# Kernel tuning notes

Hardware: AMD Instinct MI355X
Metric: run time of the kernel (lower is better)

## Reference

```python
import jax, jax.numpy as jnp
import numpy as np

B, A, DV, RNN, H = 256, 196, 2048, 1024, 512

def setup_inputs() -> dict:
    key = jax.random.key(0)
    ks = jax.random.split(key, 8)
    s = lambda d: 1.0 / np.sqrt(d)
    return {
        "h_att": jax.random.normal(ks[0], (B, RNN), jnp.float32),
        "prev_h2": jax.random.normal(ks[1], (B, RNN), jnp.float32),
        "imgs_features": jax.random.normal(ks[2], (B, A, DV), jnp.float32),
        "W_v": jax.random.normal(ks[3], (DV, H), jnp.float32) * s(DV),
        "b_v": jnp.zeros((H,), jnp.float32),
        "W_ha": jax.random.normal(ks[4], (RNN, H), jnp.float32) * s(RNN),
        "b_ha": jnp.zeros((H,), jnp.float32),
        "W_hv": jax.random.normal(ks[5], (RNN, H), jnp.float32) * s(RNN),
        "b_hv": jnp.zeros((H,), jnp.float32),
        "W_f": jax.random.normal(ks[6], (H, 1), jnp.float32) * s(H),
        "b_f": jnp.zeros((1,), jnp.float32),
    }

def reference(h_att, prev_h2, imgs_features, W_v, b_v, W_ha, b_ha, W_hv, b_hv, W_f, b_f):
    # project image regions: [B, A, H]
    p_imgs = jnp.einsum('bad,dh->bah', imgs_features, W_v) + b_v
    # project hidden states: [B, H] -> broadcast over regions
    att_hatt = h_att @ W_ha + b_ha          # [B, H]
    att_hvis = prev_h2 @ W_hv + b_hv        # [B, H]
    dot = p_imgs + att_hatt[:, None, :] + att_hvis[:, None, :]  # [B, A, H]
    # dropout is identity in eval mode
    att = (jax.nn.relu(dot) @ W_f)[..., 0] + b_f[0]  # [B, A]
    alpha = jax.nn.softmax(att, axis=1)              # [B, A]
    # weighted sum over regions -> [B, 2048]
    return jnp.einsum('bad,ba->bd', imgs_features, alpha)
```

## Files before the change

kernel.cpp:

```cpp
#include <hip/hip_runtime.h>
#include <stdint.h>

typedef float f32x4 __attribute__((ext_vector_type(4)));
typedef short s16x8 __attribute__((ext_vector_type(8)));
typedef unsigned u32x2 __attribute__((ext_vector_type(2)));

#define B_SZ 256
#define A_RG 196
#define DVD  2048
#define RNN  1024
#define H_SZ 512
#define NKT  (DVD / 32)

__device__ __forceinline__ unsigned short f2bf(float f) {
    unsigned u = __builtin_bit_cast(unsigned, f);
    u = u + 0x7FFFu + ((u >> 16) & 1u);
    return (unsigned short)(u >> 16);
}

__device__ __forceinline__ unsigned cvt2(float a, float b) {
    unsigned r;
    asm("v_cvt_pk_bf16_f32 %0, %1, %2" : "=v"(r) : "v"(a), "v"(b));
    return r;
}

__global__ __launch_bounds__(256) void k_prepW(const float* __restrict__ Wv,
                                               unsigned short* __restrict__ Wt4) {
    __shared__ float tile[64][65];
    int kb = blockIdx.x >> 3, ct = blockIdx.x & 7;
    int k0 = kb * 64, c0 = ct * 64;
    int t = threadIdx.x;
    int cl = t & 63, rq = t >> 6;
#pragma unroll
    for (int i = 0; i < 16; ++i) {
        int r = rq * 16 + i;
        tile[r][cl] = Wv[(size_t)(k0 + r) * H_SZ + c0 + cl];
    }
    __syncthreads();
    int kl = t & 63;
#pragma unroll
    for (int i = 0; i < 16; ++i) {
        int cr = rq * 16 + i;
        int col = c0 + cr;
        int k = k0 + kl;
        int f = col >> 4, lr = col & 15;
        int kt = k >> 5, g = (k >> 3) & 3, e = k & 7;
        size_t dst = ((size_t)(kt * 32 + f) * 64 + g * 16 + lr) * 8 + e;
        Wt4[dst] = f2bf(tile[kl][cr]);
    }
}

__global__ __launch_bounds__(256) void k_base(const float* __restrict__ h_att,
                                              const float* __restrict__ prev_h2,
                                              const float* __restrict__ W_ha,
                                              const float* __restrict__ b_ha,
                                              const float* __restrict__ W_hv,
                                              const float* __restrict__ b_hv,
                                              const float* __restrict__ b_v,
                                              float* __restrict__ base_g) {
    __shared__ float ha_s[4][RNN];
    __shared__ float pv_s[4][RNN];
    int bg = blockIdx.x >> 2, hg = blockIdx.x & 3;
    int t = threadIdx.x;
#pragma unroll
    for (int i = 0; i < 16; ++i) {
        int idx = i * 256 + t;
        int bl = idx >> 10, k = idx & 1023;
        ha_s[bl][k] = h_att[(size_t)(bg * 4 + bl) * RNN + k];
        pv_s[bl][k] = prev_h2[(size_t)(bg * 4 + bl) * RNN + k];
    }
    __syncthreads();
    int h = hg * 128 + (t & 127);
    int br = t >> 7;
    float aA0 = 0, aA1 = 0, aV0 = 0, aV1 = 0;
#pragma unroll 4
    for (int k = 0; k < RNN; ++k) {
        float w1 = W_ha[(size_t)k * H_SZ + h];
        float w2 = W_hv[(size_t)k * H_SZ + h];
        aA0 = fmaf(ha_s[br * 2][k],     w1, aA0);
        aA1 = fmaf(ha_s[br * 2 + 1][k], w1, aA1);
        aV0 = fmaf(pv_s[br * 2][k],     w2, aV0);
        aV1 = fmaf(pv_s[br * 2 + 1][k], w2, aV1);
    }
    float bias = b_ha[h] + b_hv[h] + b_v[h];
    base_g[(size_t)(bg * 4 + br * 2) * H_SZ + h]     = aA0 + aV0 + bias;
    base_g[(size_t)(bg * 4 + br * 2 + 1) * H_SZ + h] = aA1 + aV1 + bias;
}

__global__ __launch_bounds__(1024, 4) void k_fused(const float* __restrict__ imgs,
                                                   const unsigned short* __restrict__ Wt4,
                                                   const float* __restrict__ base_g,
                                                   const float* __restrict__ W_f,
                                                   float* __restrict__ out) {
    __shared__ __align__(16) short A_s[2][128 * 32];
    __shared__ float att_part[8][128];
    __shared__ float e_s[128];
    __shared__ float scal_r;
    __shared__ float scal_l;

    const int b = blockIdx.x;
    const int t = threadIdx.x;
    const int lane = t & 63, w = t >> 6;
    const int wm = w >> 3, wn = w & 7;
    const int lr = lane & 15, g = lane >> 4;

    const float* imgb = imgs + (size_t)b * A_RG * DVD;
    const char* Bp = (const char*)Wt4 + ((size_t)(wn * 4) * 64 + lane) * 16;

    f32x4 o2;
    float o0 = 0.f, o1 = 0.f;
    float m_run = -1e30f, l_run = 0.f;
    (void)o2;

    const int arow = t >> 3, ac = t & 7;
    const unsigned awr = (unsigned)(arow * 64 +
        ((((ac >> 1) ^ ((arow ^ (arow >> 2)) & 3)) << 4) | ((ac & 1) << 3)));

    unsigned ard[4];
#pragma unroll
    for (int mf = 0; mf < 4; ++mf) {
        int r = wm * 64 + mf * 16 + lr;
        ard[mf] = (unsigned)(r * 64 + ((g ^ ((r ^ (r >> 2)) & 3)) << 4));
    }

    for (int at = 0; at < 2; ++at) {
        const bool last = (at == 1);
        const int m0 = at * 128;

        const float* Ag = imgb + (size_t)min(m0 + arow, A_RG - 1) * DVD + ac * 4;

        f32x4 acc[4][4] = {};
        f32x4 rA;
        s16x8 aF[4], bR[4];

        auto ldA = [&](int kt) {
            rA = *(const f32x4*)(Ag + (size_t)kt * 32);
        };
        auto wrA = [&](int buf) {
            u32x2 pk;
            pk[0] = cvt2(rA[0], rA[1]);
            pk[1] = cvt2(rA[2], rA[3]);
            *(u32x2*)((char*)A_s[buf] + awr) = pk;
        };
        auto ldB = [&](int kt) {
            const char* p = Bp + (size_t)kt * 32768;
#pragma unroll
            for (int n = 0; n < 4; ++n)
                bR[n] = *(const s16x8*)(p + n * 1024);
        };

        ldB(0);
        ldA(0);
        wrA(0);
        asm volatile("s_waitcnt lgkmcnt(0)" ::: "memory");
        __builtin_amdgcn_sched_barrier(0);
        __builtin_amdgcn_s_barrier();

        for (int kt = 0; kt < NKT; ++kt) {
            if (kt + 1 < NKT) ldA(kt + 1);
            const char* Ac = (const char*)A_s[kt & 1];
#pragma unroll
            for (int mf = 0; mf < 4; ++mf)
                aF[mf] = *(const s16x8*)(Ac + ard[mf]);
            __builtin_amdgcn_s_setprio(1);
#pragma unroll
            for (int mf = 0; mf < 4; ++mf)
#pragma unroll
                for (int n = 0; n < 4; ++n)
                    acc[mf][n] = __builtin_amdgcn_mfma_f32_16x16x32_bf16(
                        aF[mf], bR[n], acc[mf][n], 0, 0, 0);
            __builtin_amdgcn_s_setprio(0);
            if (kt + 1 < NKT) {
                ldB(kt + 1);
                wrA((kt + 1) & 1);
                asm volatile("s_waitcnt lgkmcnt(0)" ::: "memory");
                __builtin_amdgcn_sched_barrier(0);
                __builtin_amdgcn_s_barrier();
            }
        }

        {
            float wfv[4], bs[4];
#pragma unroll
            for (int n = 0; n < 4; ++n) {
                int col = wn * 64 + n * 16 + lr;
                wfv[n] = W_f[col];
                bs[n] = base_g[(size_t)b * H_SZ + col];
            }
#pragma unroll
            for (int mf = 0; mf < 4; ++mf) {
                float pj[4] = {0.f, 0.f, 0.f, 0.f};
#pragma unroll
                for (int n = 0; n < 4; ++n) {
                    float a0 = fmaxf(acc[mf][n][0] + bs[n], 0.f);
                    float a1 = fmaxf(acc[mf][n][1] + bs[n], 0.f);
                    float a2 = fmaxf(acc[mf][n][2] + bs[n], 0.f);
                    float a3 = fmaxf(acc[mf][n][3] + bs[n], 0.f);
                    pj[0] = fmaf(a0, wfv[n], pj[0]);
                    pj[1] = fmaf(a1, wfv[n], pj[1]);
                    pj[2] = fmaf(a2, wfv[n], pj[2]);
                    pj[3] = fmaf(a3, wfv[n], pj[3]);
                }
#pragma unroll
                for (int j = 0; j < 4; ++j) {
                    float s = pj[j];
                    s += __shfl_xor(s, 1);
                    s += __shfl_xor(s, 2);
                    s += __shfl_xor(s, 4);
                    s += __shfl_xor(s, 8);
                    if (lr == 0)
                        att_part[wn][wm * 64 + mf * 16 + g * 4 + j] = s;
                }
            }
        }
        __builtin_amdgcn_s_barrier();

        if (w == 0) {
            int gr0 = m0 + lane, gr1 = m0 + lane + 64;
            float s0, s1;
            {
                float a = 0.f, c = 0.f;
#pragma unroll
                for (int q = 0; q < 8; ++q) {
                    a += att_part[q][lane];
                    c += att_part[q][lane + 64];
                }
                s0 = (gr0 < A_RG) ? a : -1e30f;
                s1 = (gr1 < A_RG) ? c : -1e30f;
            }
            float mx = fmaxf(s0, s1);
            for (int d = 1; d < 64; d <<= 1) mx = fmaxf(mx, __shfl_xor(mx, d));
            float m_new = fmaxf(m_run, mx);
            float r = __expf(m_run - m_new);
            float e0 = __expf(s0 - m_new);
            float e1 = __expf(s1 - m_new);
            float es = e0 + e1;
            for (int d = 1; d < 64; d <<= 1) es += __shfl_xor(es, d);
            l_run = l_run * r + es;
            m_run = m_new;
            e_s[lane] = e0;
            e_s[lane + 64] = e1;
            if (lane == 0) {
                scal_r = r;
                if (last) scal_l = l_run;
            }
        }
        __builtin_amdgcn_s_barrier();

        {
            float r = scal_r;
            o0 *= r; o1 *= r;
            const float2* vb = (const float2*)imgb + t;
            const int AV = last ? (A_RG - 128) : 128;
#pragma unroll 4
            for (int a = 0; a < AV; ++a) {
                float e = e_s[a];
                float2 v = vb[(size_t)(m0 + a) * (DVD / 2)];
                o0 = fmaf(e, v.x, o0);
                o1 = fmaf(e, v.y, o1);
            }
        }
    }

    float linv = 1.0f / scal_l;
    float2 res = make_float2(o0 * linv, o1 * linv);
    ((float2*)(out + (size_t)b * DVD))[t] = res;
}

extern "C" void kernel_launch(void* const* d_in, const int* in_sizes, int n_in,
                              void* d_out, int out_size, void* d_ws, size_t ws_size,
                              hipStream_t stream) {
    const float* h_att   = (const float*)d_in[0];
    const float* prev_h2 = (const float*)d_in[1];
    const float* imgs    = (const float*)d_in[2];
    const float* W_v     = (const float*)d_in[3];
    const float* b_v     = (const float*)d_in[4];
    const float* W_ha    = (const float*)d_in[5];
    const float* b_ha    = (const float*)d_in[6];
    const float* W_hv    = (const float*)d_in[7];
    const float* b_hv    = (const float*)d_in[8];
    const float* W_f     = (const float*)d_in[9];

    unsigned short* Wt4 = (unsigned short*)d_ws;
    float* base_g = (float*)((char*)d_ws + (size_t)DVD * H_SZ * 2);
    float* out = (float*)d_out;

    hipLaunchKernelGGL(k_prepW, dim3(256), dim3(256), 0, stream, W_v, Wt4);
    hipLaunchKernelGGL(k_base, dim3(256), dim3(256), 0, stream,
                       h_att, prev_h2, W_ha, b_ha, W_hv, b_hv, b_v, base_g);
    hipLaunchKernelGGL(k_fused, dim3(B_SZ), dim3(1024), 0, stream,
                       imgs, Wt4, base_g, W_f, out);
}
```

Before: 334.5 us.

## Quad-buffer A tile in LDS and barrier once per two k-steps

The A staging buffer in LDS grows from two to four slots. The main loop now processes k-tiles in pairs: it prefetches two A tiles ahead into separate registers, converts them to bf16 and writes them into the free slots, and issues a single wait-and-barrier per pair instead of per k-step. The aim is to halve workgroup barrier stalls and give global loads more time to land before they are needed. In exchange it uses more LDS and more vector registers for the extra prefetch, which could reduce occupancy or cause spills.

```diff
diff --git a/kernel.cpp b/kernel.cpp
--- a/kernel.cpp
+++ b/kernel.cpp
@@ -92,7 +92,7 @@
                                                    const float* __restrict__ base_g,
                                                    const float* __restrict__ W_f,
                                                    float* __restrict__ out) {
-    __shared__ __align__(16) short A_s[2][128 * 32];
+    __shared__ __align__(16) short A_s[4][128 * 32];
     __shared__ float att_part[8][128];
     __shared__ float e_s[128];
     __shared__ float scal_r;
@@ -107,10 +107,8 @@
     const float* imgb = imgs + (size_t)b * A_RG * DVD;
     const char* Bp = (const char*)Wt4 + ((size_t)(wn * 4) * 64 + lane) * 16;
 
-    f32x4 o2;
     float o0 = 0.f, o1 = 0.f;
     float m_run = -1e30f, l_run = 0.f;
-    (void)o2;
 
     const int arow = t >> 3, ac = t & 7;
     const unsigned awr = (unsigned)(arow * 64 +
@@ -130,16 +128,16 @@
         const float* Ag = imgb + (size_t)min(m0 + arow, A_RG - 1) * DVD + ac * 4;
 
         f32x4 acc[4][4] = {};
-        f32x4 rA;
-        s16x8 aF[4], bR[4];
-
-        auto ldA = [&](int kt) {
-            rA = *(const f32x4*)(Ag + (size_t)kt * 32);
-        };
-        auto wrA = [&](int buf) {
+        f32x4 rAe, rAo;
+        s16x8 bR[4];
+
+        auto ldA = [&](int kt, f32x4& r) {
+            r = *(const f32x4*)(Ag + (size_t)kt * 32);
+        };
+        auto wrA = [&](int buf, const f32x4& r) {
             u32x2 pk;
-            pk[0] = cvt2(rA[0], rA[1]);
-            pk[1] = cvt2(rA[2], rA[3]);
+            pk[0] = cvt2(r[0], r[1]);
+            pk[1] = cvt2(r[2], r[3]);
             *(u32x2*)((char*)A_s[buf] + awr) = pk;
         };
         auto ldB = [&](int kt) {
@@ -148,17 +146,9 @@
             for (int n = 0; n < 4; ++n)
                 bR[n] = *(const s16x8*)(p + n * 1024);
         };
-
-        ldB(0);
-        ldA(0);
-        wrA(0);
-        asm volatile("s_waitcnt lgkmcnt(0)" ::: "memory");
-        __builtin_amdgcn_sched_barrier(0);
-        __builtin_amdgcn_s_barrier();
-
-        for (int kt = 0; kt < NKT; ++kt) {
-            if (kt + 1 < NKT) ldA(kt + 1);
-            const char* Ac = (const char*)A_s[kt & 1];
+        auto compute = [&](int buf) {
+            const char* Ac = (const char*)A_s[buf];
+            s16x8 aF[4];
 #pragma unroll
             for (int mf = 0; mf < 4; ++mf)
                 aF[mf] = *(const s16x8*)(Ac + ard[mf]);
@@ -170,14 +160,35 @@
                     acc[mf][n] = __builtin_amdgcn_mfma_f32_16x16x32_bf16(
                         aF[mf], bR[n], acc[mf][n], 0, 0, 0);
             __builtin_amdgcn_s_setprio(0);
-            if (kt + 1 < NKT) {
-                ldB(kt + 1);
-                wrA((kt + 1) & 1);
-                asm volatile("s_waitcnt lgkmcnt(0)" ::: "memory");
-                __builtin_amdgcn_sched_barrier(0);
-                __builtin_amdgcn_s_barrier();
-            }
+        };
+        auto fence = [&]() {
+            asm volatile("s_waitcnt lgkmcnt(0)" ::: "memory");
+            __builtin_amdgcn_sched_barrier(0);
+            __builtin_amdgcn_s_barrier();
+        };
+
+        ldB(0);
+        ldA(0, rAe);
+        wrA(0, rAe);
+        ldA(1, rAo);
+        wrA(1, rAo);
+        fence();
+
+        for (int gp = 0; gp < NKT / 2 - 1; ++gp) {
+            const int kt0 = 2 * gp, kt1 = 2 * gp + 1;
+            ldA(kt0 + 2, rAe);
+            ldA(kt1 + 2, rAo);
+            compute(kt0 & 3);
+            ldB(kt0 + 1);
+            wrA((kt0 + 2) & 3, rAe);
+            compute(kt1 & 3);
+            ldB(kt1 + 1);
+            wrA((kt1 + 2) & 3, rAo);
+            fence();
         }
+        compute(2);
+        ldB(NKT - 1);
+        compute(3);
 
         {
             float wfv[4], bs[4];
```

After: 357.2 us. 6.8% more time.

## Stream A and B tiles into LDS via global_load_lds with deeper pipelining

Applied to the files above, without the earlier changes.

Image fp32 tiles are now loaded straight into a 4-stage LDS ring with global_load_lds and converted to bf16 at fragment-read time, replacing the register load / convert / ds_write path. Projection weights are also staged through a double-buffered LDS region instead of per-wave register loads. Waits move to vmcnt-based synchronisation so that two A tiles and one B tile can be in flight. This is meant to hide global latency and cut VGPR staging. In exchange, LDS use grows to about 128KB per block, which likely limits each CU to one block, and the fp32 LDS reads double LDS traffic for A.

```diff
diff --git a/kernel.cpp b/kernel.cpp
--- a/kernel.cpp
+++ b/kernel.cpp
@@ -3,7 +3,7 @@
 
 typedef float f32x4 __attribute__((ext_vector_type(4)));
 typedef short s16x8 __attribute__((ext_vector_type(8)));
-typedef unsigned u32x2 __attribute__((ext_vector_type(2)));
+typedef unsigned u32x4 __attribute__((ext_vector_type(4)));
 
 #define B_SZ 256
 #define A_RG 196
@@ -22,6 +22,12 @@
     unsigned r;
     asm("v_cvt_pk_bf16_f32 %0, %1, %2" : "=v"(r) : "v"(a), "v"(b));
     return r;
+}
+
+__device__ __forceinline__ void gll16(const void* g, void* l) {
+    __builtin_amdgcn_global_load_lds(
+        (const __attribute__((address_space(1))) void*)g,
+        (__attribute__((address_space(3))) void*)l, 16, 0, 0);
 }
 
 __global__ __launch_bounds__(256) void k_prepW(const float* __restrict__ Wv,
@@ -92,7 +98,8 @@
                                                    const float* __restrict__ base_g,
                                                    const float* __restrict__ W_f,
                                                    float* __restrict__ out) {
-    __shared__ __align__(16) short A_s[2][128 * 32];
+    __shared__ __align__(16) float A_s[4][128 * 32];
+    __shared__ __align__(16) short B_s[2][H_SZ * 32];
     __shared__ float att_part[8][128];
     __shared__ float e_s[128];
     __shared__ float scal_r;
@@ -105,75 +112,93 @@
     const int lr = lane & 15, g = lane >> 4;
 
     const float* imgb = imgs + (size_t)b * A_RG * DVD;
-    const char* Bp = (const char*)Wt4 + ((size_t)(wn * 4) * 64 + lane) * 16;
-
-    f32x4 o2;
+
+    const char* Bg = (const char*)Wt4 + (size_t)w * 2048 + (size_t)lane * 16;
+    const unsigned Bld = (unsigned)(w * 2048 + lane * 16);
+    unsigned brd[4];
+#pragma unroll
+    for (int n = 0; n < 4; ++n)
+        brd[n] = (unsigned)((wn * 4 + n) * 1024 + lane * 16);
+
+    unsigned aLo[4], aHi[4];
+#pragma unroll
+    for (int mf = 0; mf < 4; ++mf) {
+        int r = wm * 64 + mf * 16 + lr;
+        aLo[mf] = (unsigned)(r * 128 + (((2 * g)     ^ (r & 7)) << 4));
+        aHi[mf] = (unsigned)(r * 128 + (((2 * g + 1) ^ (r & 7)) << 4));
+    }
+
+    const int slr = lane >> 3;
+    const int sch = (lane & 7) ^ slr;
+    const unsigned Ald = (unsigned)(w * 1024 + lane * 16);
+
     float o0 = 0.f, o1 = 0.f;
     float m_run = -1e30f, l_run = 0.f;
-    (void)o2;
-
-    const int arow = t >> 3, ac = t & 7;
-    const unsigned awr = (unsigned)(arow * 64 +
-        ((((ac >> 1) ^ ((arow ^ (arow >> 2)) & 3)) << 4) | ((ac & 1) << 3)));
-
-    unsigned ard[4];
-#pragma unroll
-    for (int mf = 0; mf < 4; ++mf) {
-        int r = wm * 64 + mf * 16 + lr;
-        ard[mf] = (unsigned)(r * 64 + ((g ^ ((r ^ (r >> 2)) & 3)) << 4));
-    }
 
     for (int at = 0; at < 2; ++at) {
         const bool last = (at == 1);
         const int m0 = at * 128;
 
-        const float* Ag = imgb + (size_t)min(m0 + arow, A_RG - 1) * DVD + ac * 4;
+        const char* AgB = (const char*)(imgb
+            + (size_t)min(m0 + w * 8 + slr, A_RG - 1) * DVD) + sch * 16;
 
         f32x4 acc[4][4] = {};
-        f32x4 rA;
-        s16x8 aF[4], bR[4];
-
-        auto ldA = [&](int kt) {
-            rA = *(const f32x4*)(Ag + (size_t)kt * 32);
+
+        auto stA = [&](int kt) {
+            gll16(AgB + (size_t)kt * 128, (char*)A_s[kt & 3] + Ald);
         };
-        auto wrA = [&](int buf) {
-            u32x2 pk;
-            pk[0] = cvt2(rA[0], rA[1]);
-            pk[1] = cvt2(rA[2], rA[3]);
-            *(u32x2*)((char*)A_s[buf] + awr) = pk;
+        auto stB = [&](int kt) {
+            const char* s = Bg + (size_t)kt * 32768;
+            char* d = (char*)B_s[kt & 1] + Bld;
+            gll16(s, d);
+            gll16(s + 1024, d + 1024);
         };
-        auto ldB = [&](int kt) {
-            const char* p = Bp + (size_t)kt * 32768;
+        auto compute = [&](int kt) {
+            const char* Ac = (const char*)A_s[kt & 3];
+            const char* Bc = (const char*)B_s[kt & 1];
+            s16x8 aF[4], bq[4];
+#pragma unroll
+            for (int mf = 0; mf < 4; ++mf) {
+                f32x4 lo = *(const f32x4*)(Ac + aLo[mf]);
+                f32x4 hi = *(const f32x4*)(Ac + aHi[mf]);
+                u32x4 pk;
+                pk[0] = cvt2(lo[0], lo[1]);
+                pk[1] = cvt2(lo[2], lo[3]);
+                pk[2] = cvt2(hi[0], hi[1]);
+                pk[3] = cvt2(hi[2], hi[3]);
+                aF[mf] = __builtin_bit_cast(s16x8, pk);
+            }
 #pragma unroll
             for (int n = 0; n < 4; ++n)
-                bR[n] = *(const s16x8*)(p + n * 1024);
+                bq[n] = *(const s16x8*)(Bc + brd[n]);
+            __builtin_amdgcn_s_setprio(1);
+#pragma unroll
+            for (int mf = 0; mf < 4; ++mf)
+#pragma unroll
+                for (int n = 0; n < 4; ++n)
+                    acc[mf][n] = __builtin_amdgcn_mfma_f32_16x16x32_bf16(
+                        aF[mf], bq[n], acc[mf][n], 0, 0, 0);
+            __builtin_amdgcn_s_setprio(0);
         };
 
-        ldB(0);
-        ldA(0);
-        wrA(0);
-        asm volatile("s_waitcnt lgkmcnt(0)" ::: "memory");
+        stB(0);
+        stA(0);
+        stA(1);
+        asm volatile("s_waitcnt vmcnt(0)" ::: "memory");
         __builtin_amdgcn_sched_barrier(0);
         __builtin_amdgcn_s_barrier();
 
         for (int kt = 0; kt < NKT; ++kt) {
-            if (kt + 1 < NKT) ldA(kt + 1);
-            const char* Ac = (const char*)A_s[kt & 1];
-#pragma unroll
-            for (int mf = 0; mf < 4; ++mf)
-                aF[mf] = *(const s16x8*)(Ac + ard[mf]);
-            __builtin_amdgcn_s_setprio(1);
-#pragma unroll
-            for (int mf = 0; mf < 4; ++mf)
-#pragma unroll
-                for (int n = 0; n < 4; ++n)
-                    acc[mf][n] = __builtin_amdgcn_mfma_f32_16x16x32_bf16(
-                        aF[mf], bR[n], acc[mf][n], 0, 0, 0);
-            __builtin_amdgcn_s_setprio(0);
+            if (kt + 1 < NKT) stB(kt + 1);
+            if (kt + 2 < NKT) stA(kt + 2);
+            __builtin_amdgcn_sched_barrier(0);
+            compute(kt);
+            __builtin_amdgcn_sched_barrier(0);
             if (kt + 1 < NKT) {
-                ldB(kt + 1);
-                wrA((kt + 1) & 1);
-                asm volatile("s_waitcnt lgkmcnt(0)" ::: "memory");
+                if (kt + 2 < NKT)
+                    asm volatile("s_waitcnt vmcnt(1) lgkmcnt(0)" ::: "memory");
+                else
+                    asm volatile("s_waitcnt vmcnt(0) lgkmcnt(0)" ::: "memory");
                 __builtin_amdgcn_sched_barrier(0);
                 __builtin_amdgcn_s_barrier();
             }
```

Result: slower. 391.8 us (+17.1%).
